# Performance work log

Measured on AMD Instinct MI355X. Metric: run time of the kernel, lower is better.

## Reference

```python
import jax, jax.numpy as jnp
import numpy as np

EPS = 1e-8  # torch.nn.CosineSimilarity default eps


def setup_inputs() -> dict:
    key = jax.random.key(0)
    k1, k2 = jax.random.split(key)
    B, D = 2048, 512
    return {
        "z_i": jax.random.normal(k1, (B, D), dtype=jnp.float32),
        "z_j": jax.random.normal(k2, (B, D), dtype=jnp.float32),
        "temperature": 0.5,
    }


def _neg_mask_indices(B):
    # static (numpy) mask: remove diagonal and the two +/-B positive diagonals
    N = 2 * B
    mask = np.ones((N, N), dtype=bool)
    np.fill_diagonal(mask, False)
    idx = np.arange(B)
    mask[idx, idx + B] = False
    mask[idx + B, idx] = False
    rows, cols = np.where(mask)  # each row keeps exactly N-2 entries, row-major order
    return rows, cols


def reference(z_i, z_j, temperature):
    B = z_i.shape[0]
    N = 2 * B
    z = jnp.concatenate([z_i, z_j], axis=0)                      # [N, D]
    # cosine similarity = normalized GEMM (same math as pairwise CosineSimilarity)
    zn = z / jnp.maximum(jnp.linalg.norm(z, axis=1, keepdims=True), EPS)
    sim = jnp.matmul(zn, zn.T) / temperature                      # [N, N]

    pos = jnp.concatenate([jnp.diagonal(sim, B), jnp.diagonal(sim, -B)])[:, None]  # [N, 1]
    rows, cols = _neg_mask_indices(B)
    neg = sim[rows, cols].reshape(N, N - 2)                       # [N, N-2]

    logits = jnp.concatenate([pos, neg], axis=1)                  # [N, N-1], label = 0
    # sum-reduced cross-entropy with label 0, divided by N
    loss = jnp.sum(jax.nn.logsumexp(logits, axis=1) - logits[:, 0]) / N

    # avg_rank: position of the positive (column 0) in descending sort of logits
    order = jnp.argsort(-logits, axis=1)
    avg_rank = jnp.mean(jnp.argmin(order, axis=1).astype(jnp.float32))
    return loss, avg_rank
```

## Files before the change

### kernel.cpp

```cpp
#include <hip/hip_runtime.h>
#include <math.h>

#define DDIM 512
#define THREADS 256
#define BT 128
#define BK 64
#define NT 32
#define NTILES (NT * (NT + 1) / 2)
#define NCH 64

typedef __attribute__((ext_vector_type(8))) __bf16 bf16x8;
typedef __attribute__((ext_vector_type(4))) float f32x4;
typedef __attribute__((ext_vector_type(8))) unsigned short ushort8;

__device__ __forceinline__ float bf2f(unsigned short u) {
  union { unsigned int i; float f; } v; v.i = ((unsigned int)u) << 16; return v.f;
}
__device__ __forceinline__ unsigned short f2bf(float f) {
  unsigned int u = __builtin_bit_cast(unsigned int, f);
  return (unsigned short)((u + 0x7fffu + ((u >> 16) & 1u)) >> 16);
}

#define GLOAD_LDS16(gp, lp)                                                   \
  __builtin_amdgcn_global_load_lds(                                           \
      (const __attribute__((address_space(1))) unsigned int*)(gp),            \
      (__attribute__((address_space(3))) unsigned int*)(lp), 16, 0, 0)

__global__ void k_prep(const float* __restrict__ zi, const float* __restrict__ zj,
                       const float* __restrict__ tempp,
                       unsigned short* __restrict__ znb, float* __restrict__ pos,
                       int B) {
  int wv = (blockIdx.x * blockDim.x + threadIdx.x) >> 6;
  int lane = threadIdx.x & 63;
  if (wv >= B) return;
  const float* a = zi + (size_t)wv * DDIM;
  const float* b = zj + (size_t)wv * DDIM;
  float4 a0 = *(const float4*)(a + lane * 8);
  float4 a1 = *(const float4*)(a + lane * 8 + 4);
  float4 b0 = *(const float4*)(b + lane * 8);
  float4 b1 = *(const float4*)(b + lane * 8 + 4);
  float av[8] = {a0.x, a0.y, a0.z, a0.w, a1.x, a1.y, a1.z, a1.w};
  float bv[8] = {b0.x, b0.y, b0.z, b0.w, b1.x, b1.y, b1.z, b1.w};
  float sa = 0.f, sb = 0.f;
#pragma unroll
  for (int i = 0; i < 8; ++i) { sa = fmaf(av[i], av[i], sa); sb = fmaf(bv[i], bv[i], sb); }
#pragma unroll
  for (int off = 32; off; off >>= 1) { sa += __shfl_xor(sa, off, 64); sb += __shfl_xor(sb, off, 64); }
  float ia = 1.f / fmaxf(sqrtf(sa), 1e-8f);
  float ib = 1.f / fmaxf(sqrtf(sb), 1e-8f);
  ushort8 ua, ub;
  float fa[8], fb[8];
#pragma unroll
  for (int i = 0; i < 8; ++i) {
    unsigned short x = f2bf(av[i] * ia); ua[i] = x; fa[i] = bf2f(x);
    unsigned short y = f2bf(bv[i] * ib); ub[i] = y; fb[i] = bf2f(y);
  }
  *(ushort8*)(znb + (size_t)wv * DDIM + lane * 8) = ua;
  *(ushort8*)(znb + (size_t)(wv + B) * DDIM + lane * 8) = ub;
  float pd = 0.f;
#pragma unroll
  for (int i = 0; i < 8; ++i) pd = fmaf(fa[i], fb[i], pd);
#pragma unroll
  for (int off = 32; off; off >>= 1) pd += __shfl_xor(pd, off, 64);
  if (lane == 0) {
    float p = pd / tempp[0];
    pos[wv] = p; pos[wv + B] = p;
  }
}

__device__ __forceinline__ void stage_tile(const unsigned short* __restrict__ znb,
                                           int panel0, int k0, unsigned char* dst,
                                           int wave, int lane) {
  const int srow_in = lane >> 3;
  const int slog = (lane & 7) ^ srow_in;
#pragma unroll
  for (int j = 0; j < 4; ++j) {
    const int ww = wave * 4 + j;
    const int row = 8 * ww + srow_in;
    GLOAD_LDS16(znb + (size_t)(panel0 + row) * DDIM + k0 + slog * 8, dst + ww * 1024);
  }
}

__global__ __launch_bounds__(THREADS, 4) void k_main(
    const unsigned short* __restrict__ znb, const float* __restrict__ pos,
    const float* __restrict__ tempp, float* __restrict__ partS,
    float* __restrict__ partC, int B) {
  int tri = (blockIdx.x & 7) * (NTILES / 8) + (blockIdx.x >> 3);
  int bi = 0;
  while (tri >= NT - bi) { tri -= NT - bi; ++bi; }
  const int bj = bi + tri;
  const int r0 = bi * BT, c0 = bj * BT;
  const bool diag = (bi == bj);
  const float invt = 1.0f / tempp[0];

  __shared__ __align__(16) unsigned char sA[BT * BK * 2];
  __shared__ __align__(16) unsigned char sB[BT * BK * 2];

  const int t = threadIdx.x;
  const int lane = t & 63;
  const int wave = t >> 6;
  const int wr = wave >> 1, wc = wave & 1;
  const int cl = lane & 15, g = lane >> 4;

  f32x4 acc[4][4];
#pragma unroll
  for (int m = 0; m < 4; ++m)
#pragma unroll
    for (int n = 0; n < 4; ++n) acc[m][n] = (f32x4){0.f, 0.f, 0.f, 0.f};

  for (int kt = 0; kt < DDIM / BK; ++kt) {
    stage_tile(znb, r0, kt * BK, sA, wave, lane);
    if (!diag) stage_tile(znb, c0, kt * BK, sB, wave, lane);
    __syncthreads();

    const unsigned char* pA = sA;
    const unsigned char* pB = diag ? sA : sB;
#pragma unroll
    for (int ks = 0; ks < 2; ++ks) {
      const int phys = (g + ks * 4) ^ (cl & 7);
      bf16x8 aF[4], bF[4];
#pragma unroll
      for (int m = 0; m < 4; ++m)
        aF[m] = *(const bf16x8*)(pA + (wr * 64 + m * 16 + cl) * 128 + phys * 16);
#pragma unroll
      for (int n = 0; n < 4; ++n)
        bF[n] = *(const bf16x8*)(pB + (wc * 64 + n * 16 + cl) * 128 + phys * 16);
#pragma unroll
      for (int m = 0; m < 4; ++m)
#pragma unroll
        for (int n = 0; n < 4; ++n)
          acc[m][n] = __builtin_amdgcn_mfma_f32_16x16x32_bf16(aF[m], bF[n], acc[m][n], 0, 0, 0);
    }
    if (kt + 1 < DDIM / BK)
      __syncthreads();
  }

  int growv[16], gpartr[16];
  float pvr[16];
#pragma unroll
  for (int m = 0; m < 4; ++m)
#pragma unroll
    for (int reg = 0; reg < 4; ++reg) {
      int idx = m * 4 + reg;
      int grow = r0 + wr * 64 + m * 16 + g * 4 + reg;
      growv[idx] = grow;
      gpartr[idx] = (grow < B) ? grow + B : grow - B;
      pvr[idx] = pos[grow];
    }
  int gcolv[4], gpartc[4];
  float pvc[4];
#pragma unroll
  for (int n = 0; n < 4; ++n) {
    int gcol = c0 + wc * 64 + n * 16 + cl;
    gcolv[n] = gcol;
    gpartc[n] = (gcol < B) ? gcol + B : gcol - B;
    pvc[n] = pos[gcol];
  }

  float ssr[16], ccr[16], ssc[4], ccc[4];
#pragma unroll
  for (int i = 0; i < 16; ++i) { ssr[i] = 0.f; ccr[i] = 0.f; }
#pragma unroll
  for (int n = 0; n < 4; ++n) { ssc[n] = 0.f; ccc[n] = 0.f; }

#pragma unroll
  for (int m = 0; m < 4; ++m)
#pragma unroll
    for (int n = 0; n < 4; ++n)
#pragma unroll
      for (int reg = 0; reg < 4; ++reg) {
        const int idx = m * 4 + reg;
        float val = acc[m][n][reg] * invt;
        float e = __expf(val);
        bool isd = diag && (gcolv[n] == growv[idx]);
        if (!isd) {
          ssr[idx] += e;
          ccr[idx] += (gcolv[n] != gpartr[idx] && val > pvr[idx]) ? 1.f : 0.f;
        }
        if (!diag) {
          ssc[n] += e;
          ccc[n] += (growv[idx] != gpartc[n] && val > pvc[n]) ? 1.f : 0.f;
        }
      }

  const int chR = bj * 2 + wc;
#pragma unroll
  for (int idx = 0; idx < 16; ++idx) {
    float s = ssr[idx], c = ccr[idx];
#pragma unroll
    for (int off = 1; off < 16; off <<= 1) {
      s += __shfl_xor(s, off, 64);
      c += __shfl_xor(c, off, 64);
    }
    if (cl == 0) {
      partS[(size_t)growv[idx] * NCH + chR] = s;
      partC[(size_t)growv[idx] * NCH + chR] = c;
    }
  }
  if (!diag) {
    const int chC = bi * 2 + wr;
#pragma unroll
    for (int n = 0; n < 4; ++n) {
      float s = ssc[n], c = ccc[n];
      s += __shfl_xor(s, 16, 64); c += __shfl_xor(c, 16, 64);
      s += __shfl_xor(s, 32, 64); c += __shfl_xor(c, 32, 64);
      if (g == 0) {
        partS[(size_t)gcolv[n] * NCH + chC] = s;
        partC[(size_t)gcolv[n] * NCH + chC] = c;
      }
    }
  }
}

__global__ void k_rowfin(const float* __restrict__ partS, const float* __restrict__ partC,
                         const float* __restrict__ pos, float* __restrict__ rowL,
                         float* __restrict__ rowC, int N) {
  int r = (blockIdx.x * blockDim.x + threadIdx.x) >> 6;
  int lane = threadIdx.x & 63;
  if (r >= N) return;
  float s = partS[(size_t)r * NCH + lane];
  float c = partC[(size_t)r * NCH + lane];
#pragma unroll
  for (int off = 32; off; off >>= 1) { s += __shfl_xor(s, off, 64); c += __shfl_xor(c, off, 64); }
  if (lane == 0) {
    rowL[r] = logf(s) - pos[r];
    rowC[r] = c;
  }
}

__global__ void k_final(const float* __restrict__ rowL, const float* __restrict__ rowC,
                        float* __restrict__ out, int N) {
  float ls = 0.f, cs = 0.f;
  for (int r = threadIdx.x; r < N; r += THREADS) { ls += rowL[r]; cs += rowC[r]; }
  __shared__ float l[THREADS], c[THREADS];
  l[threadIdx.x] = ls; c[threadIdx.x] = cs;
  __syncthreads();
  for (int off = THREADS / 2; off; off >>= 1) {
    if (threadIdx.x < off) { l[threadIdx.x] += l[threadIdx.x + off]; c[threadIdx.x] += c[threadIdx.x + off]; }
    __syncthreads();
  }
  if (threadIdx.x == 0) { out[0] = l[0] / (float)N; out[1] = c[0] / (float)N; }
}

extern "C" void kernel_launch(void* const* d_in, const int* in_sizes, int n_in,
                              void* d_out, int out_size, void* d_ws, size_t ws_size,
                              hipStream_t stream) {
  const float* zi = (const float*)d_in[0];
  const float* zj = (const float*)d_in[1];
  const float* temp = (const float*)d_in[2];
  float* out = (float*)d_out;

  const int B = in_sizes[0] / DDIM;
  const int N = 2 * B;

  unsigned short* znb = (unsigned short*)d_ws;
  float* fws = (float*)(znb + (size_t)N * DDIM);
  float* pos   = fws;
  float* partS = pos + N;
  float* partC = partS + (size_t)N * NCH;
  float* rowL  = partC + (size_t)N * NCH;
  float* rowC  = rowL + N;

  k_prep<<<(B * 64) / THREADS, THREADS, 0, stream>>>(zi, zj, temp, znb, pos, B);
  k_main<<<NTILES, THREADS, 0, stream>>>(znb, pos, temp, partS, partC, B);
  k_rowfin<<<(N * 64) / THREADS, THREADS, 0, stream>>>(partS, partC, pos, rowL, rowC, N);
  k_final<<<1, THREADS, 0, stream>>>(rowL, rowC, out, N);
}
```

Before: 50.63 us.

## Shrink similarity tiles to 64x64 and merge partial sums through LDS

Measured after the change: 43.10 us. 14.9% less time.

```diff
diff --git a/kernel.cpp b/kernel.cpp
--- a/kernel.cpp
+++ b/kernel.cpp
@@ -3,9 +3,9 @@
 
 #define DDIM 512
 #define THREADS 256
-#define BT 128
+#define BT 64
 #define BK 64
-#define NT 32
+#define NT 64
 #define NTILES (NT * (NT + 1) / 2)
 #define NCH 64
 
@@ -74,14 +74,14 @@
   const int srow_in = lane >> 3;
   const int slog = (lane & 7) ^ srow_in;
 #pragma unroll
-  for (int j = 0; j < 4; ++j) {
-    const int ww = wave * 4 + j;
+  for (int j = 0; j < 2; ++j) {
+    const int ww = wave * 2 + j;
     const int row = 8 * ww + srow_in;
     GLOAD_LDS16(znb + (size_t)(panel0 + row) * DDIM + k0 + slog * 8, dst + ww * 1024);
   }
 }
 
-__global__ __launch_bounds__(THREADS, 4) void k_main(
+__global__ __launch_bounds__(THREADS) void k_main(
     const unsigned short* __restrict__ znb, const float* __restrict__ pos,
     const float* __restrict__ tempp, float* __restrict__ partS,
     float* __restrict__ partC, int B) {
@@ -102,11 +102,11 @@
   const int wr = wave >> 1, wc = wave & 1;
   const int cl = lane & 15, g = lane >> 4;
 
-  f32x4 acc[4][4];
-#pragma unroll
-  for (int m = 0; m < 4; ++m)
-#pragma unroll
-    for (int n = 0; n < 4; ++n) acc[m][n] = (f32x4){0.f, 0.f, 0.f, 0.f};
+  f32x4 acc[2][2];
+#pragma unroll
+  for (int m = 0; m < 2; ++m)
+#pragma unroll
+    for (int n = 0; n < 2; ++n) acc[m][n] = (f32x4){0.f, 0.f, 0.f, 0.f};
 
   for (int kt = 0; kt < DDIM / BK; ++kt) {
     stage_tile(znb, r0, kt * BK, sA, wave, lane);
@@ -118,55 +118,54 @@
 #pragma unroll
     for (int ks = 0; ks < 2; ++ks) {
       const int phys = (g + ks * 4) ^ (cl & 7);
-      bf16x8 aF[4], bF[4];
-#pragma unroll
-      for (int m = 0; m < 4; ++m)
-        aF[m] = *(const bf16x8*)(pA + (wr * 64 + m * 16 + cl) * 128 + phys * 16);
-#pragma unroll
-      for (int n = 0; n < 4; ++n)
-        bF[n] = *(const bf16x8*)(pB + (wc * 64 + n * 16 + cl) * 128 + phys * 16);
-#pragma unroll
-      for (int m = 0; m < 4; ++m)
-#pragma unroll
-        for (int n = 0; n < 4; ++n)
+      bf16x8 aF[2], bF[2];
+#pragma unroll
+      for (int m = 0; m < 2; ++m)
+        aF[m] = *(const bf16x8*)(pA + (wr * 32 + m * 16 + cl) * 128 + phys * 16);
+#pragma unroll
+      for (int n = 0; n < 2; ++n)
+        bF[n] = *(const bf16x8*)(pB + (wc * 32 + n * 16 + cl) * 128 + phys * 16);
+#pragma unroll
+      for (int m = 0; m < 2; ++m)
+#pragma unroll
+        for (int n = 0; n < 2; ++n)
           acc[m][n] = __builtin_amdgcn_mfma_f32_16x16x32_bf16(aF[m], bF[n], acc[m][n], 0, 0, 0);
     }
-    if (kt + 1 < DDIM / BK)
-      __syncthreads();
-  }
-
-  int growv[16], gpartr[16];
-  float pvr[16];
-#pragma unroll
-  for (int m = 0; m < 4; ++m)
+    __syncthreads();
+  }
+
+  int growv[8], gpartr[8];
+  float pvr[8];
+#pragma unroll
+  for (int m = 0; m < 2; ++m)
 #pragma unroll
     for (int reg = 0; reg < 4; ++reg) {
       int idx = m * 4 + reg;
-      int grow = r0 + wr * 64 + m * 16 + g * 4 + reg;
+      int grow = r0 + wr * 32 + m * 16 + g * 4 + reg;
       growv[idx] = grow;
       gpartr[idx] = (grow < B) ? grow + B : grow - B;
       pvr[idx] = pos[grow];
     }
-  int gcolv[4], gpartc[4];
-  float pvc[4];
-#pragma unroll
-  for (int n = 0; n < 4; ++n) {
-    int gcol = c0 + wc * 64 + n * 16 + cl;
+  int gcolv[2], gpartc[2];
+  float pvc[2];
+#pragma unroll
+  for (int n = 0; n < 2; ++n) {
+    int gcol = c0 + wc * 32 + n * 16 + cl;
     gcolv[n] = gcol;
     gpartc[n] = (gcol < B) ? gcol + B : gcol - B;
     pvc[n] = pos[gcol];
   }
 
-  float ssr[16], ccr[16], ssc[4], ccc[4];
-#pragma unroll
-  for (int i = 0; i < 16; ++i) { ssr[i] = 0.f; ccr[i] = 0.f; }
-#pragma unroll
-  for (int n = 0; n < 4; ++n) { ssc[n] = 0.f; ccc[n] = 0.f; }
-
-#pragma unroll
-  for (int m = 0; m < 4; ++m)
-#pragma unroll
-    for (int n = 0; n < 4; ++n)
+  float ssr[8], ccr[8], ssc[2], ccc[2];
+#pragma unroll
+  for (int i = 0; i < 8; ++i) { ssr[i] = 0.f; ccr[i] = 0.f; }
+#pragma unroll
+  for (int n = 0; n < 2; ++n) { ssc[n] = 0.f; ccc[n] = 0.f; }
+
+#pragma unroll
+  for (int m = 0; m < 2; ++m)
+#pragma unroll
+    for (int n = 0; n < 2; ++n)
 #pragma unroll
       for (int reg = 0; reg < 4; ++reg) {
         const int idx = m * 4 + reg;
@@ -183,32 +182,57 @@
         }
       }
 
-  const int chR = bj * 2 + wc;
-#pragma unroll
-  for (int idx = 0; idx < 16; ++idx) {
-    float s = ssr[idx], c = ccr[idx];
+#pragma unroll
+  for (int idx = 0; idx < 8; ++idx) {
 #pragma unroll
     for (int off = 1; off < 16; off <<= 1) {
-      s += __shfl_xor(s, off, 64);
-      c += __shfl_xor(c, off, 64);
-    }
-    if (cl == 0) {
-      partS[(size_t)growv[idx] * NCH + chR] = s;
-      partC[(size_t)growv[idx] * NCH + chR] = c;
-    }
-  }
-  if (!diag) {
-    const int chC = bi * 2 + wr;
-#pragma unroll
-    for (int n = 0; n < 4; ++n) {
-      float s = ssc[n], c = ccc[n];
-      s += __shfl_xor(s, 16, 64); c += __shfl_xor(c, 16, 64);
-      s += __shfl_xor(s, 32, 64); c += __shfl_xor(c, 32, 64);
-      if (g == 0) {
-        partS[(size_t)gcolv[n] * NCH + chC] = s;
-        partC[(size_t)gcolv[n] * NCH + chC] = c;
+      ssr[idx] += __shfl_xor(ssr[idx], off, 64);
+      ccr[idx] += __shfl_xor(ccr[idx], off, 64);
+    }
+  }
+#pragma unroll
+  for (int n = 0; n < 2; ++n) {
+    ssc[n] += __shfl_xor(ssc[n], 16, 64); ccc[n] += __shfl_xor(ccc[n], 16, 64);
+    ssc[n] += __shfl_xor(ssc[n], 32, 64); ccc[n] += __shfl_xor(ccc[n], 32, 64);
+  }
+
+  __syncthreads();
+  float* rowSb = (float*)sA;
+  float* rowCb = rowSb + 128;
+  float* colSb = rowSb + 256;
+  float* colCb = rowSb + 384;
+  if (cl == 0) {
+#pragma unroll
+    for (int m = 0; m < 2; ++m)
+#pragma unroll
+      for (int reg = 0; reg < 4; ++reg) {
+        int idx = m * 4 + reg;
+        int r32 = wr * 32 + m * 16 + g * 4 + reg;
+        rowSb[r32 * 2 + wc] = ssr[idx];
+        rowCb[r32 * 2 + wc] = ccr[idx];
       }
-    }
+  }
+  if (!diag && g == 0) {
+#pragma unroll
+    for (int n = 0; n < 2; ++n) {
+      int c32 = wc * 32 + n * 16 + cl;
+      colSb[c32 * 2 + wr] = ssc[n];
+      colCb[c32 * 2 + wr] = ccc[n];
+    }
+  }
+  __syncthreads();
+
+  if (wc == 0 && lane < 32) {
+    int r32 = wr * 32 + lane;
+    int r = r0 + r32;
+    partS[(size_t)r * NCH + bj] = rowSb[r32 * 2] + rowSb[r32 * 2 + 1];
+    partC[(size_t)r * NCH + bj] = rowCb[r32 * 2] + rowCb[r32 * 2 + 1];
+  }
+  if (!diag && wr == 0 && lane < 32) {
+    int c32 = wc * 32 + lane;
+    int c = c0 + c32;
+    partS[(size_t)c * NCH + bi] = colSb[c32 * 2] + colSb[c32 * 2 + 1];
+    partC[(size_t)c * NCH + bi] = colCb[c32 * 2] + colCb[c32 * 2 + 1];
   }
 }
 
```

## Shrink tiles to 64x64, keep A rows in registers, reduce columns via LDS

Applied to the files above, without the earlier changes.

After: 53.87 us. 1.06x slower.

```diff
diff --git a/kernel.cpp b/kernel.cpp
--- a/kernel.cpp
+++ b/kernel.cpp
@@ -3,9 +3,9 @@
 
 #define DDIM 512
 #define THREADS 256
-#define BT 128
+#define BT 64
 #define BK 64
-#define NT 32
+#define NT 64
 #define NTILES (NT * (NT + 1) / 2)
 #define NCH 64
 
@@ -74,14 +74,14 @@
   const int srow_in = lane >> 3;
   const int slog = (lane & 7) ^ srow_in;
 #pragma unroll
-  for (int j = 0; j < 4; ++j) {
-    const int ww = wave * 4 + j;
+  for (int j = 0; j < 2; ++j) {
+    const int ww = wave * 2 + j;
     const int row = 8 * ww + srow_in;
     GLOAD_LDS16(znb + (size_t)(panel0 + row) * DDIM + k0 + slog * 8, dst + ww * 1024);
   }
 }
 
-__global__ __launch_bounds__(THREADS, 4) void k_main(
+__global__ __launch_bounds__(THREADS) void k_main(
     const unsigned short* __restrict__ znb, const float* __restrict__ pos,
     const float* __restrict__ tempp, float* __restrict__ partS,
     float* __restrict__ partC, int B) {
@@ -93,121 +93,116 @@
   const bool diag = (bi == bj);
   const float invt = 1.0f / tempp[0];
 
-  __shared__ __align__(16) unsigned char sA[BT * BK * 2];
   __shared__ __align__(16) unsigned char sB[BT * BK * 2];
 
   const int t = threadIdx.x;
   const int lane = t & 63;
   const int wave = t >> 6;
-  const int wr = wave >> 1, wc = wave & 1;
   const int cl = lane & 15, g = lane >> 4;
 
-  f32x4 acc[4][4];
-#pragma unroll
-  for (int m = 0; m < 4; ++m)
-#pragma unroll
-    for (int n = 0; n < 4; ++n) acc[m][n] = (f32x4){0.f, 0.f, 0.f, 0.f};
-
+  const unsigned short* aBase = znb + (size_t)(r0 + wave * 16 + cl) * DDIM + g * 8;
+  bf16x8 aR[16];
+#pragma unroll
+  for (int s = 0; s < 16; ++s)
+    aR[s] = *(const bf16x8*)(aBase + s * 32);
+
+  f32x4 acc[4];
+#pragma unroll
+  for (int n = 0; n < 4; ++n) acc[n] = (f32x4){0.f, 0.f, 0.f, 0.f};
+
+#pragma unroll
   for (int kt = 0; kt < DDIM / BK; ++kt) {
-    stage_tile(znb, r0, kt * BK, sA, wave, lane);
-    if (!diag) stage_tile(znb, c0, kt * BK, sB, wave, lane);
-    __syncthreads();
-
-    const unsigned char* pA = sA;
-    const unsigned char* pB = diag ? sA : sB;
+    stage_tile(znb, c0, kt * BK, sB, wave, lane);
+    __syncthreads();
 #pragma unroll
     for (int ks = 0; ks < 2; ++ks) {
       const int phys = (g + ks * 4) ^ (cl & 7);
-      bf16x8 aF[4], bF[4];
-#pragma unroll
-      for (int m = 0; m < 4; ++m)
-        aF[m] = *(const bf16x8*)(pA + (wr * 64 + m * 16 + cl) * 128 + phys * 16);
+      bf16x8 bF[4];
 #pragma unroll
       for (int n = 0; n < 4; ++n)
-        bF[n] = *(const bf16x8*)(pB + (wc * 64 + n * 16 + cl) * 128 + phys * 16);
-#pragma unroll
-      for (int m = 0; m < 4; ++m)
-#pragma unroll
-        for (int n = 0; n < 4; ++n)
-          acc[m][n] = __builtin_amdgcn_mfma_f32_16x16x32_bf16(aF[m], bF[n], acc[m][n], 0, 0, 0);
-    }
-    if (kt + 1 < DDIM / BK)
-      __syncthreads();
-  }
-
-  int growv[16], gpartr[16];
-  float pvr[16];
-#pragma unroll
-  for (int m = 0; m < 4; ++m)
-#pragma unroll
-    for (int reg = 0; reg < 4; ++reg) {
-      int idx = m * 4 + reg;
-      int grow = r0 + wr * 64 + m * 16 + g * 4 + reg;
-      growv[idx] = grow;
-      gpartr[idx] = (grow < B) ? grow + B : grow - B;
-      pvr[idx] = pos[grow];
-    }
+        bF[n] = *(const bf16x8*)(sB + (n * 16 + cl) * 128 + phys * 16);
+#pragma unroll
+      for (int n = 0; n < 4; ++n)
+        acc[n] = __builtin_amdgcn_mfma_f32_16x16x32_bf16(aR[kt * 2 + ks], bF[n], acc[n], 0, 0, 0);
+    }
+    __syncthreads();
+  }
+
+  int growv[4], gpartr[4];
+  float pvr[4];
+#pragma unroll
+  for (int reg = 0; reg < 4; ++reg) {
+    int grow = r0 + wave * 16 + g * 4 + reg;
+    growv[reg] = grow;
+    gpartr[reg] = (grow < B) ? grow + B : grow - B;
+    pvr[reg] = pos[grow];
+  }
   int gcolv[4], gpartc[4];
   float pvc[4];
 #pragma unroll
   for (int n = 0; n < 4; ++n) {
-    int gcol = c0 + wc * 64 + n * 16 + cl;
+    int gcol = c0 + n * 16 + cl;
     gcolv[n] = gcol;
     gpartc[n] = (gcol < B) ? gcol + B : gcol - B;
     pvc[n] = pos[gcol];
   }
 
-  float ssr[16], ccr[16], ssc[4], ccc[4];
-#pragma unroll
-  for (int i = 0; i < 16; ++i) { ssr[i] = 0.f; ccr[i] = 0.f; }
-#pragma unroll
-  for (int n = 0; n < 4; ++n) { ssc[n] = 0.f; ccc[n] = 0.f; }
-
-#pragma unroll
-  for (int m = 0; m < 4; ++m)
-#pragma unroll
-    for (int n = 0; n < 4; ++n)
-#pragma unroll
-      for (int reg = 0; reg < 4; ++reg) {
-        const int idx = m * 4 + reg;
-        float val = acc[m][n][reg] * invt;
-        float e = __expf(val);
-        bool isd = diag && (gcolv[n] == growv[idx]);
-        if (!isd) {
-          ssr[idx] += e;
-          ccr[idx] += (gcolv[n] != gpartr[idx] && val > pvr[idx]) ? 1.f : 0.f;
-        }
-        if (!diag) {
-          ssc[n] += e;
-          ccc[n] += (growv[idx] != gpartc[n] && val > pvc[n]) ? 1.f : 0.f;
-        }
+  float ssr[4], ccr[4], ssc[4], ccc[4];
+#pragma unroll
+  for (int i = 0; i < 4; ++i) { ssr[i] = 0.f; ccr[i] = 0.f; ssc[i] = 0.f; ccc[i] = 0.f; }
+
+#pragma unroll
+  for (int n = 0; n < 4; ++n)
+#pragma unroll
+    for (int reg = 0; reg < 4; ++reg) {
+      float val = acc[n][reg] * invt;
+      float e = __expf(val);
+      bool isd = diag && (gcolv[n] == growv[reg]);
+      if (!isd) {
+        ssr[reg] += e;
+        ccr[reg] += (gcolv[n] != gpartr[reg] && val > pvr[reg]) ? 1.f : 0.f;
       }
-
-  const int chR = bj * 2 + wc;
-#pragma unroll
-  for (int idx = 0; idx < 16; ++idx) {
-    float s = ssr[idx], c = ccr[idx];
+      if (!diag) {
+        ssc[n] += e;
+        ccc[n] += (growv[reg] != gpartc[n] && val > pvc[n]) ? 1.f : 0.f;
+      }
+    }
+
+#pragma unroll
+  for (int reg = 0; reg < 4; ++reg) {
+    float s = ssr[reg], c = ccr[reg];
 #pragma unroll
     for (int off = 1; off < 16; off <<= 1) {
       s += __shfl_xor(s, off, 64);
       c += __shfl_xor(c, off, 64);
     }
     if (cl == 0) {
-      partS[(size_t)growv[idx] * NCH + chR] = s;
-      partC[(size_t)growv[idx] * NCH + chR] = c;
-    }
-  }
+      partS[(size_t)growv[reg] * NCH + bj] = s;
+      partC[(size_t)growv[reg] * NCH + bj] = c;
+    }
+  }
+
   if (!diag) {
-    const int chC = bi * 2 + wr;
 #pragma unroll
     for (int n = 0; n < 4; ++n) {
-      float s = ssc[n], c = ccc[n];
-      s += __shfl_xor(s, 16, 64); c += __shfl_xor(c, 16, 64);
-      s += __shfl_xor(s, 32, 64); c += __shfl_xor(c, 32, 64);
-      if (g == 0) {
-        partS[(size_t)gcolv[n] * NCH + chC] = s;
-        partC[(size_t)gcolv[n] * NCH + chC] = c;
+      ssc[n] += __shfl_xor(ssc[n], 16, 64); ccc[n] += __shfl_xor(ccc[n], 16, 64);
+      ssc[n] += __shfl_xor(ssc[n], 32, 64); ccc[n] += __shfl_xor(ccc[n], 32, 64);
+    }
+    float* colS = (float*)sB;
+    float* colC = colS + 256;
+    if (g == 0) {
+#pragma unroll
+      for (int n = 0; n < 4; ++n) {
+        colS[wave * 64 + n * 16 + cl] = ssc[n];
+        colC[wave * 64 + n * 16 + cl] = ccc[n];
       }
+    }
+    __syncthreads();
+    if (t < 64) {
+      float s = colS[t] + colS[64 + t] + colS[128 + t] + colS[192 + t];
+      float c = colC[t] + colC[64 + t] + colC[128 + t] + colC[192 + t];
+      partS[(size_t)(c0 + t) * NCH + bi] = s;
+      partC[(size_t)(c0 + t) * NCH + bi] = c;
     }
   }
 }
```
